# Kernel optimization log

Measured on AMD Instinct MI355X. Metric: run time of the kernel, lower is better.

The kernel has to match this reference:

```python
import jax, jax.numpy as jnp
import numpy as np

H = 2048      # hidden_size
NH = 32       # num attention heads
KVH = 8       # num kv heads
HD = 64       # head_dim
G = NH // KVH # kv groups (4)
EPS = 1e-6
THETA = 1000000.0


def _rms_norm(x, g):
    # normalize over last dim (head_dim)
    var = jnp.mean(jnp.square(x), axis=-1, keepdims=True)
    return x * jax.lax.rsqrt(var + EPS) * g


def _rope(seq_len, dtype):
    inv_freq = 1.0 / (THETA ** (jnp.arange(0, HD, 2, dtype=jnp.float32) / HD))
    pos = jnp.arange(seq_len, dtype=jnp.float32)
    freqs = pos[:, None] * inv_freq[None, :]          # [S, HD/2]
    emb = jnp.concatenate([freqs, freqs], axis=-1)    # [S, HD]
    return jnp.cos(emb).astype(dtype), jnp.sin(emb).astype(dtype)


def _rotate_half(x):
    x1, x2 = jnp.split(x, 2, axis=-1)
    return jnp.concatenate([-x2, x1], axis=-1)


def setup_inputs() -> dict:
    key = jax.random.key(0)
    ks = jax.random.split(key, 8)
    B, S = 1, 2048
    s = lambda fan_in: 1.0 / np.sqrt(fan_in)
    return {
        "hidden_states": jax.random.normal(ks[0], (B, S, H), jnp.float32),
        "Wq": jax.random.normal(ks[1], (H, NH * HD + NH), jnp.float32) * s(H),
        "Wk": jax.random.normal(ks[2], (H, KVH * HD), jnp.float32) * s(H),
        "Wv": jax.random.normal(ks[3], (H, KVH * HD), jnp.float32) * s(H),
        "Wo": jax.random.normal(ks[4], (NH * HD, H), jnp.float32) * s(NH * HD),
        "g_q": jnp.ones((HD,), jnp.float32),
        "g_k": jnp.ones((HD,), jnp.float32),
    }


def reference(hidden_states, Wq, Wk, Wv, Wo, g_q, g_k):
    B, S, _ = hidden_states.shape
    dtype = hidden_states.dtype

    qg = hidden_states @ Wq                              # [B,S,NH*HD+NH]
    k = hidden_states @ Wk                               # [B,S,KVH*HD]
    v = hidden_states @ Wv

    # headwise gate split, grouped per kv head (matches torch view/split)
    qg = qg.reshape(B, S, KVH, G * HD + G)
    q, gate = qg[..., : G * HD], qg[..., G * HD :]       # gate: [B,S,KVH,G]
    gate = gate.reshape(B, S, NH, 1)
    q = q.reshape(B, S, NH, HD).transpose(0, 2, 1, 3)    # [B,NH,S,HD]
    k = k.reshape(B, S, KVH, HD).transpose(0, 2, 1, 3)   # [B,KVH,S,HD]
    v = v.reshape(B, S, KVH, HD).transpose(0, 2, 1, 3)

    q = _rms_norm(q, g_q)
    k = _rms_norm(k, g_k)

    cos, sin = _rope(S, dtype)                           # [S,HD]
    cos, sin = cos[None, None], sin[None, None]
    q = q * cos + _rotate_half(q) * sin
    k = k * cos + _rotate_half(k) * sin

    # GQA: repeat kv heads
    k = jnp.repeat(k, G, axis=1)                         # [B,NH,S,HD]
    v = jnp.repeat(v, G, axis=1)

    # causal SDPA
    scale = 1.0 / np.sqrt(HD)
    scores = jnp.einsum("bhqd,bhkd->bhqk", q, k) * scale
    causal = jnp.tril(jnp.ones((S, S), bool))
    scores = jnp.where(causal[None, None], scores, jnp.finfo(dtype).min)
    probs = jax.nn.softmax(scores, axis=-1)
    attn = jnp.einsum("bhqk,bhkd->bhqd", probs, v)       # [B,NH,S,HD]

    attn = attn.transpose(0, 2, 1, 3)                    # [B,S,NH,HD]
    attn = attn * jax.nn.sigmoid(gate)
    attn = attn.reshape(B, S, NH * HD)
    return attn @ Wo
```

## Files before the change

kernel.cpp:

```cpp
#include <hip/hip_runtime.h>
#include <hip/hip_bf16.h>

#define SLEN 2048
#define HDIM 2048
#define NHEAD 32
#define KVHEAD 8
#define HEADD 64
#define NTOT 3104
#define NPAD 3200

typedef short bh8 __attribute__((ext_vector_type(8)));
typedef float f32x4 __attribute__((ext_vector_type(4)));

#define QSCALE 0.1803368801111204f

__device__ __forceinline__ unsigned short f2bf(float f) {
    union { float f; unsigned int u; } v; v.f = f;
    unsigned int u = v.u;
    return (unsigned short)((u + 0x7fffu + ((u >> 16) & 1u)) >> 16);
}

__device__ __forceinline__ unsigned int cvtpk_bf16(float lo, float hi) {
    unsigned int r;
    asm("v_cvt_pk_bf16_f32 %0, %1, %2" : "=v"(r) : "v"(lo), "v"(hi));
    return r;
}

__device__ __forceinline__ void gl_lds16(const unsigned short* g, unsigned short* l) {
    __builtin_amdgcn_global_load_lds(
        (const __attribute__((address_space(1))) unsigned int*)g,
        (__attribute__((address_space(3))) unsigned int*)l, 16, 0, 0);
}

__global__ void cast_x_k(const float* __restrict__ src, unsigned short* __restrict__ dst, int n) {
    int i = blockIdx.x * blockDim.x + threadIdx.x;
    int base = i * 4;
    if (base < n) {
        float4 f = *(const float4*)(src + base);
        ushort4 o;
        o.x = f2bf(f.x); o.y = f2bf(f.y); o.z = f2bf(f.z); o.w = f2bf(f.w);
        *(ushort4*)(dst + base) = o;
    }
}

__global__ void pack_wt_k(const float* __restrict__ Wq, const float* __restrict__ Wk,
                          const float* __restrict__ Wv, unsigned short* __restrict__ Wt) {
    __shared__ float tile[32][33];
    int n0 = blockIdx.x * 32, k0 = blockIdx.y * 32;
    int t = threadIdx.x;
    for (int i = 0; i < 4; i++) {
        int idx = i * 256 + t;
        int kr = idx >> 5, nc = idx & 31;
        int n = n0 + nc, k = k0 + kr;
        float val = 0.f;
        if (n < 2048)       { int h = n >> 6, d = n & 63; val = Wq[(size_t)k * 2080 + (h >> 2) * 260 + (h & 3) * 64 + d]; }
        else if (n < 2080)  { int h = n - 2048;           val = Wq[(size_t)k * 2080 + (h >> 2) * 260 + 256 + (h & 3)]; }
        else if (n < 2592)  { val = Wk[(size_t)k * 512 + (n - 2080)]; }
        else if (n < 3104)  { val = Wv[(size_t)k * 512 + (n - 2592)]; }
        tile[kr][nc] = val;
    }
    __syncthreads();
    for (int i = 0; i < 4; i++) {
        int idx = i * 256 + t;
        int nr = idx >> 5, kc = idx & 31;
        Wt[(size_t)(n0 + nr) * HDIM + (k0 + kc)] = f2bf(tile[kc][nr]);
    }
}

__global__ void pack_wot_k(const float* __restrict__ Wo, unsigned short* __restrict__ Wt) {
    __shared__ float tile[32][33];
    int n0 = blockIdx.x * 32, k0 = blockIdx.y * 32;
    int t = threadIdx.x;
    for (int i = 0; i < 4; i++) {
        int idx = i * 256 + t;
        int kr = idx >> 5, nc = idx & 31;
        tile[kr][nc] = Wo[(size_t)(k0 + kr) * 2048 + (n0 + nc)];
    }
    __syncthreads();
    for (int i = 0; i < 4; i++) {
        int idx = i * 256 + t;
        int nr = idx >> 5, kc = idx & 31;
        Wt[(size_t)(n0 + nr) * 2048 + (k0 + kc)] = f2bf(tile[kc][nr]);
    }
}

template<int NST>
__global__ __launch_bounds__(256) void gemm_nt64_k(const unsigned short* __restrict__ A,
                                                   const unsigned short* __restrict__ Bt,
                                                   float* __restrict__ C0,
                                                   float* __restrict__ C1,
                                                   int ldc, int mtiles, int ntiles) {
    const int K = 2048;
    __shared__ unsigned short As[3][64 * 32];
    __shared__ unsigned short Bs[3][128 * 32];
    int d = blockIdx.x;
    int nwg = gridDim.x;
    int cpx = nwg >> 3;
    int swz = (d & 7) * cpx + (d >> 3);
    int half = (swz >= ntiles) ? 1 : 0;
    int tile = swz - half * ntiles;
    int m0 = (tile % mtiles) * 64, n0 = (tile / mtiles) * 128;
    float* C = half ? C1 : C0;
    int koff = half * (NST * 32);
    int t = threadIdx.x;
    int w = t >> 6, l = t & 63;
    int wm = (w >> 1) * 32, wn = (w & 1) * 64;
    int lrow = l & 15, lc = l >> 4;
    int rsw = (lrow >> 1) & 3;
    int scol = ((l & 3) ^ ((l >> 3) & 3)) * 8;

    f32x4 acc[2][4];
    #pragma unroll
    for (int i = 0; i < 2; i++)
        #pragma unroll
        for (int j = 0; j < 4; j++)
            acc[i][j] = {0.f, 0.f, 0.f, 0.f};

    const unsigned short* ga = &A[(size_t)(m0 + w * 16 + (l >> 2)) * K + koff + scol];
    const unsigned short* gb = &Bt[(size_t)(n0 + w * 32 + (l >> 2)) * K + koff + scol];

#define STAGE_NT64(s, b) do { \
        gl_lds16(ga + (size_t)(s) * 32,                  &As[b][w * 512]); \
        gl_lds16(gb + (size_t)(s) * 32,                  &Bs[b][(w * 2 + 0) * 512]); \
        gl_lds16(gb + (size_t)(s) * 32 + 16 * (size_t)K, &Bs[b][(w * 2 + 1) * 512]); \
    } while (0)

#define GBODY(rb) do { \
        bh8 af[2], bb[4]; \
        _Pragma("unroll") \
        for (int i = 0; i < 2; i++) \
            af[i] = *(const bh8*)(&As[rb][(wm + i * 16 + lrow) * 32 + ((lc ^ rsw) * 8)]); \
        _Pragma("unroll") \
        for (int j = 0; j < 4; j++) \
            bb[j] = *(const bh8*)(&Bs[rb][(wn + j * 16 + lrow) * 32 + ((lc ^ rsw) * 8)]); \
        _Pragma("unroll") \
        for (int i = 0; i < 2; i++) \
            _Pragma("unroll") \
            for (int j = 0; j < 4; j++) \
                acc[i][j] = __builtin_amdgcn_mfma_f32_16x16x32_bf16(af[i], bb[j], acc[i][j], 0, 0, 0); \
    } while (0)

#define WB3 asm volatile("s_waitcnt vmcnt(3)\n\ts_barrier" ::: "memory")

    STAGE_NT64(0, 0);
    STAGE_NT64(1, 1);
    if constexpr (NST == 64) {
        for (int sb = 0; sb < 60; sb += 3) {
            WB3;
            STAGE_NT64(sb + 2, 2);
            GBODY(0);
            WB3;
            STAGE_NT64(sb + 3, 0);
            GBODY(1);
            WB3;
            STAGE_NT64(sb + 4, 1);
            GBODY(2);
        }
        WB3;
        STAGE_NT64(62, 2);
        GBODY(0);
        WB3;
        STAGE_NT64(63, 0);
        GBODY(1);
        WB3;
        GBODY(2);
        asm volatile("s_waitcnt vmcnt(0)\n\ts_barrier" ::: "memory");
        GBODY(0);
    } else {
        for (int sb = 0; sb < 30; sb += 3) {
            WB3;
            STAGE_NT64(sb + 2, 2);
            GBODY(0);
            WB3;
            STAGE_NT64(sb + 3, 0);
            GBODY(1);
            WB3;
            STAGE_NT64(sb + 4, 1);
            GBODY(2);
        }
        WB3;
        GBODY(0);
        asm volatile("s_waitcnt vmcnt(0)\n\ts_barrier" ::: "memory");
        GBODY(1);
    }
#undef WB3
#undef STAGE_NT64
#undef GBODY
    int col = l & 15, rbase = (l >> 4) * 4;
    for (int i = 0; i < 2; i++)
        for (int j = 0; j < 4; j++)
            #pragma unroll
            for (int r = 0; r < 4; r++)
                C[(size_t)(m0 + wm + i * 16 + rbase + r) * ldc + (n0 + wn + j * 16 + col)] = acc[i][j][r];
}

__global__ void addf4_k(const float* __restrict__ a, const float* __restrict__ b,
                        float* __restrict__ o) {
    int i = (blockIdx.x * 256 + threadIdx.x) * 4;
    float4 x = *(const float4*)(a + i);
    float4 y = *(const float4*)(b + i);
    float4 r; r.x = x.x + y.x; r.y = x.y + y.y; r.z = x.z + y.z; r.w = x.w + y.w;
    *(float4*)(o + i) = r;
}

__global__ void post_qkv_k(const float* __restrict__ QKVG,
                           unsigned short* __restrict__ Qr, unsigned short* __restrict__ Kr,
                           unsigned short* __restrict__ Vt, float* __restrict__ gate,
                           const float* __restrict__ g_q, const float* __restrict__ g_k) {
    __shared__ float tile[64][65];
    int b = blockIdx.x;
    if (b < 20480) {
        int wid = b * 4 + (threadIdx.x >> 6);
        int lane = threadIdx.x & 63;
        int type, s, hh;
        if (wid < SLEN * NHEAD) { type = 0; s = wid >> 5; hh = wid & 31; }
        else                    { int r = wid - SLEN * NHEAD; type = 1; s = r >> 3; hh = r & 7; }
        int col = (type == 0) ? hh * 64 + lane : 2080 + hh * 64 + lane;
        float x = QKVG[(size_t)s * NPAD + col];
        float sq = x * x;
        #pragma unroll
        for (int off = 32; off; off >>= 1) sq += __shfl_xor(sq, off);
        float inv = rsqrtf(sq * (1.f / 64.f) + 1e-6f);
        float g = (type == 0 ? g_q : g_k)[lane];
        float xn = x * inv * g;
        float xp = __shfl_xor(xn, 32);
        float xr = (lane < 32) ? -xp : xp;
        int i = lane & 31;
        float invf = __expf(-(float)i * (0.03125f * 13.815510557964274f));
        float ang = (float)s * invf;
        float c = cosf(ang), sn = sinf(ang);
        float r = xn * c + xr * sn;
        if (type == 0) Qr[((size_t)hh * SLEN + s) * 64 + lane] = f2bf(r * QSCALE);
        else           Kr[((size_t)hh * SLEN + s) * 64 + lane] = f2bf(r);
    } else if (b < 20736) {
        int b2 = b - 20480;
        int hh = b2 >> 5, s0 = (b2 & 31) * 64;
        int t = threadIdx.x;
        #pragma unroll
        for (int i = 0; i < 4; i++) {
            int idx = i * 256 + t;
            int sr = idx >> 4, c4 = (idx & 15) * 4;
            float4 f = *(const float4*)(&QKVG[(size_t)(s0 + sr) * NPAD + 2592 + hh * 64 + c4]);
            tile[sr][c4] = f.x; tile[sr][c4 + 1] = f.y; tile[sr][c4 + 2] = f.z; tile[sr][c4 + 3] = f.w;
        }
        __syncthreads();
        #pragma unroll
        for (int i = 0; i < 4; i++) {
            int idx = i * 256 + t;
            int dr = idx >> 4, c4 = (idx & 15) * 4;
            int hb = c4 >> 5, f = (c4 >> 4) & 1, g = (c4 >> 2) & 3;
            int p = (hb * 4 + g) * 8 + f * 4;
            ushort4 o;
            o.x = f2bf(tile[c4][dr]); o.y = f2bf(tile[c4 + 1][dr]);
            o.z = f2bf(tile[c4 + 2][dr]); o.w = f2bf(tile[c4 + 3][dr]);
            *(ushort4*)(&Vt[((size_t)hh * 64 + dr) * SLEN + s0 + p]) = o;
        }
    } else {
        int b2 = b - 20736;
        int i = b2 * 256 + threadIdx.x;
        int s = i >> 5, h = i & 31;
        float x = QKVG[(size_t)s * NPAD + 2048 + h];
        gate[i] = 1.f / (1.f + __expf(-x));
    }
}

__global__ __launch_bounds__(256) void attn_k(const unsigned short* __restrict__ Qr,
                                              const unsigned short* __restrict__ Kr,
                                              const unsigned short* __restrict__ Vt,
                                              const float* __restrict__ gate,
                                              unsigned short* __restrict__ attn) {
    __shared__ unsigned short Kls[3][64 * 64];
    __shared__ unsigned short Vls[3][64 * 64];
    int d = blockIdx.x;
    int kvh = d & 7;
    int h = kvh * 4 + ((d >> 3) & 3);
    int qt = 31 - (d >> 5);
    int t = threadIdx.x, w = t >> 6, l = t & 63;
    int ql = l & 15, g = l >> 4;
    const float NEGINF = -__builtin_inff();

    const unsigned short* Kh = Kr + (size_t)kvh * SLEN * 64;
    const unsigned short* Vh = Vt + (size_t)kvh * 64 * SLEN;
    const unsigned short* Qh = Qr + (size_t)h * SLEN * 64;
    int lk = g * 8;
    int r8 = l >> 3, c8 = l & 7;
    int cs = 8 * (c8 ^ r8);
    int R0 = w * 16, R1 = w * 16 + 8;
    int rdswz = (ql & 7) << 4;

    int q0 = qt * 64;
    int qrow = q0 + w * 16 + ql;

    bh8 qa0 = *(const bh8*)(Qh + (size_t)qrow * 64 + lk);
    bh8 qa1 = *(const bh8*)(Qh + (size_t)qrow * 64 + 32 + lk);

    f32x4 o[4];
    #pragma unroll
    for (int i = 0; i < 4; i++) o[i] = {0.f, 0.f, 0.f, 0.f};
    float m2 = NEGINF, lsum = 0.f;

    int ntiles = qt + 1;
    {
        gl_lds16(&Kh[(size_t)(0 + R0 + r8) * 64 + cs], &Kls[0][R0 * 64]);
        gl_lds16(&Kh[(size_t)(0 + R1 + r8) * 64 + cs], &Kls[0][R1 * 64]);
        gl_lds16(&Vh[(size_t)(R0 + r8) * SLEN + 0 + cs], &Vls[0][R0 * 64]);
        gl_lds16(&Vh[(size_t)(R1 + r8) * SLEN + 0 + cs], &Vls[0][R1 * 64]);
    }
    if (ntiles > 1) {
        gl_lds16(&Kh[(size_t)(64 + R0 + r8) * 64 + cs], &Kls[1][R0 * 64]);
        gl_lds16(&Kh[(size_t)(64 + R1 + r8) * 64 + cs], &Kls[1][R1 * 64]);
        gl_lds16(&Vh[(size_t)(R0 + r8) * SLEN + 64 + cs], &Vls[1][R0 * 64]);
        gl_lds16(&Vh[(size_t)(R1 + r8) * SLEN + 64 + cs], &Vls[1][R1 * 64]);
    }
    int rd = 0, wr = 2;

    for (int ti = 0; ti < ntiles; ti++) {
        if (ti + 1 < ntiles) asm volatile("s_waitcnt vmcnt(4)\n\ts_barrier" ::: "memory");
        else                 asm volatile("s_waitcnt vmcnt(0)\n\ts_barrier" ::: "memory");
        if (ti + 2 < ntiles) {
            int kv1 = (ti + 2) * 64;
            gl_lds16(&Kh[(size_t)(kv1 + R0 + r8) * 64 + cs], &Kls[wr][R0 * 64]);
            gl_lds16(&Kh[(size_t)(kv1 + R1 + r8) * 64 + cs], &Kls[wr][R1 * 64]);
            gl_lds16(&Vh[(size_t)(R0 + r8) * SLEN + kv1 + cs], &Vls[wr][R0 * 64]);
            gl_lds16(&Vh[(size_t)(R1 + r8) * SLEN + kv1 + cs], &Vls[wr][R1 * 64]);
        }
        const unsigned short* Kb = &Kls[rd][0];
        const unsigned short* Vb = &Vls[rd][0];
        int kv0 = ti * 64;
        f32x4 sct[4];
        __builtin_amdgcn_s_setprio(1);
        #pragma unroll
        for (int nt = 0; nt < 4; nt++) {
            int rb = (nt * 16 + ql) * 128;
            bh8 kb0 = *(const bh8*)(&Kb[(rb + ((g * 16) ^ rdswz)) >> 1]);
            bh8 kb1 = *(const bh8*)(&Kb[(rb + ((64 + g * 16) ^ rdswz)) >> 1]);
            f32x4 a = {0.f, 0.f, 0.f, 0.f};
            a = __builtin_amdgcn_mfma_f32_16x16x32_bf16(kb0, qa0, a, 0, 0, 0);
            a = __builtin_amdgcn_mfma_f32_16x16x32_bf16(kb1, qa1, a, 0, 0, 0);
            sct[nt] = a;
        }
        __builtin_amdgcn_s_setprio(0);
        if (ti == qt) {
            #pragma unroll
            for (int nt = 0; nt < 4; nt++)
                #pragma unroll
                for (int j = 0; j < 4; j++) {
                    int key = kv0 + nt * 16 + 4 * g + j;
                    if (key > qrow) sct[nt][j] = NEGINF;
                }
        }
        float mt0 = fmaxf(fmaxf(sct[0][0], sct[0][1]), fmaxf(sct[0][2], sct[0][3]));
        float mt1 = fmaxf(fmaxf(sct[1][0], sct[1][1]), fmaxf(sct[1][2], sct[1][3]));
        float mt2 = fmaxf(fmaxf(sct[2][0], sct[2][1]), fmaxf(sct[2][2], sct[2][3]));
        float mt3 = fmaxf(fmaxf(sct[3][0], sct[3][1]), fmaxf(sct[3][2], sct[3][3]));
        float mt = fmaxf(fmaxf(mt0, mt1), fmaxf(mt2, mt3));
        mt = fmaxf(mt, __shfl_xor(mt, 16));
        mt = fmaxf(mt, __shfl_xor(mt, 32));
        if (!__all(mt - m2 <= 8.f)) {
            float mnew = fmaxf(m2, mt);
            float resc = __builtin_amdgcn_exp2f(m2 - mnew);
            m2 = mnew;
            lsum *= resc;
            float rf[4];
            #pragma unroll
            for (int j = 0; j < 4; j++) rf[j] = __shfl(resc, 4 * g + j);
            #pragma unroll
            for (int nt = 0; nt < 4; nt++) {
                f32x4 oo = o[nt];
                #pragma unroll
                for (int j = 0; j < 4; j++) oo[j] *= rf[j];
                o[nt] = oo;
            }
        }
        float ps = 0.f;
        #pragma unroll
        for (int nt = 0; nt < 4; nt++)
            #pragma unroll
            for (int j = 0; j < 4; j++) {
                float p = __builtin_amdgcn_exp2f(sct[nt][j] - m2);
                sct[nt][j] = p;
                ps += p;
            }
        ps += __shfl_xor(ps, 16);
        ps += __shfl_xor(ps, 32);
        lsum += ps;
        union { unsigned int u[4]; bh8 v; } pa0, pa1;
        pa0.u[0] = cvtpk_bf16(sct[0][0], sct[0][1]);
        pa0.u[1] = cvtpk_bf16(sct[0][2], sct[0][3]);
        pa0.u[2] = cvtpk_bf16(sct[1][0], sct[1][1]);
        pa0.u[3] = cvtpk_bf16(sct[1][2], sct[1][3]);
        pa1.u[0] = cvtpk_bf16(sct[2][0], sct[2][1]);
        pa1.u[1] = cvtpk_bf16(sct[2][2], sct[2][3]);
        pa1.u[2] = cvtpk_bf16(sct[3][0], sct[3][1]);
        pa1.u[3] = cvtpk_bf16(sct[3][2], sct[3][3]);
        __builtin_amdgcn_s_setprio(1);
        #pragma unroll
        for (int nt = 0; nt < 4; nt++) {
            int rb = (nt * 16 + ql) * 128;
            bh8 vb0 = *(const bh8*)(&Vb[(rb + ((g * 16) ^ rdswz)) >> 1]);
            bh8 vb1 = *(const bh8*)(&Vb[(rb + ((64 + g * 16) ^ rdswz)) >> 1]);
            o[nt] = __builtin_amdgcn_mfma_f32_16x16x32_bf16(pa0.v, vb0, o[nt], 0, 0, 0);
            o[nt] = __builtin_amdgcn_mfma_f32_16x16x32_bf16(pa1.v, vb1, o[nt], 0, 0, 0);
        }
        __builtin_amdgcn_s_setprio(0);
        rd = (rd == 2) ? 0 : rd + 1;
        wr = (wr == 2) ? 0 : wr + 1;
    }

    float gf[4];
    #pragma unroll
    for (int j = 0; j < 4; j++) {
        float ls = __shfl(lsum, 4 * g + j);
        int row = q0 + w * 16 + 4 * g + j;
        gf[j] = gate[row * 32 + h] / ls;
    }
    #pragma unroll
    for (int j = 0; j < 4; j++) {
        int row = q0 + w * 16 + 4 * g + j;
        #pragma unroll
        for (int nt = 0; nt < 4; nt++)
            attn[(size_t)row * 2048 + h * 64 + nt * 16 + ql] = f2bf(o[nt][j] * gf[j]);
    }
}

extern "C" void kernel_launch(void* const* d_in, const int* in_sizes, int n_in,
                              void* d_out, int out_size, void* d_ws, size_t ws_size,
                              hipStream_t stream) {
    const float* hidden = (const float*)d_in[0];
    const float* Wq = (const float*)d_in[1];
    const float* Wk = (const float*)d_in[2];
    const float* Wv = (const float*)d_in[3];
    const float* Wo = (const float*)d_in[4];
    const float* gq = (const float*)d_in[5];
    const float* gk = (const float*)d_in[6];
    float* out = (float*)d_out;
    char* ws = (char*)d_ws;

    unsigned short* X     = (unsigned short*)(ws + 0);
    unsigned short* Wt    = (unsigned short*)(ws + 8388608);
    float*          QKVG  = (float*)(ws + 21495808);
    unsigned short* Qr    = (unsigned short*)(ws + 47710208);
    unsigned short* Kr    = (unsigned short*)(ws + 56098816);
    unsigned short* Vt    = (unsigned short*)(ws + 58195968);
    float*          gate  = (float*)(ws + 60293120);
    unsigned short* attnb = (unsigned short*)(ws + 60555264);
    unsigned short* Wot   = (unsigned short*)(ws + 68943872);
    float*          P1    = (float*)(ws + 77332480);
    float*          P0    = QKVG;

    cast_x_k<<<dim3(4096), dim3(256), 0, stream>>>(hidden, X, SLEN * HDIM);
    pack_wt_k<<<dim3(100, 64), dim3(256), 0, stream>>>(Wq, Wk, Wv, Wt);
    pack_wot_k<<<dim3(64, 64), dim3(256), 0, stream>>>(Wo, Wot);
    gemm_nt64_k<64><<<dim3(800), dim3(256), 0, stream>>>(X, Wt, QKVG, QKVG, NPAD, 32, 800);
    post_qkv_k<<<dim3(20992), dim3(256), 0, stream>>>(QKVG, Qr, Kr, Vt, gate, gq, gk);
    attn_k<<<dim3(1024), dim3(256), 0, stream>>>(Qr, Kr, Vt, gate, attnb);
    gemm_nt64_k<32><<<dim3(1024), dim3(256), 0, stream>>>(attnb, Wot, P0, P1, 2048, 32, 512);
    addf4_k<<<dim3(4096), dim3(256), 0, stream>>>(P0, P1, out);
}
```

Measured before the change: 169.9 us.

## Fuse QK RMSNorm, RoPE and gate sigmoid into QKV GEMM epilogue

Reorders the packed weight columns so Q, K, V and gate land on 128-wide tile boundaries. The QKV GEMM epilogue then applies RMSNorm, RoPE and scaling directly from accumulators and writes bf16 Q/K, and computes the gate sigmoid in place. Only V is still stored in fp32 and transposed by a smaller separate kernel. This removes the fp32 round trip of Q/K/gate through global memory and a large post-processing launch, at the cost of heavier epilogue work with scattered 2-byte stores and per-element sin/cos.

```diff
diff --git a/kernel.cpp b/kernel.cpp
--- a/kernel.cpp
+++ b/kernel.cpp
@@ -54,9 +54,9 @@
         int n = n0 + nc, k = k0 + kr;
         float val = 0.f;
         if (n < 2048)       { int h = n >> 6, d = n & 63; val = Wq[(size_t)k * 2080 + (h >> 2) * 260 + (h & 3) * 64 + d]; }
-        else if (n < 2080)  { int h = n - 2048;           val = Wq[(size_t)k * 2080 + (h >> 2) * 260 + 256 + (h & 3)]; }
-        else if (n < 2592)  { val = Wk[(size_t)k * 512 + (n - 2080)]; }
-        else if (n < 3104)  { val = Wv[(size_t)k * 512 + (n - 2592)]; }
+        else if (n < 2560)  { val = Wk[(size_t)k * 512 + (n - 2048)]; }
+        else if (n < 3072)  { val = Wv[(size_t)k * 512 + (n - 2560)]; }
+        else if (n < 3104)  { int h = n - 3072;           val = Wq[(size_t)k * 2080 + (h >> 2) * 260 + 256 + (h & 3)]; }
         tile[kr][nc] = val;
     }
     __syncthreads();
@@ -84,12 +84,17 @@
     }
 }
 
-template<int NST>
+template<int NST, bool FUSE>
 __global__ __launch_bounds__(256) void gemm_nt64_k(const unsigned short* __restrict__ A,
                                                    const unsigned short* __restrict__ Bt,
                                                    float* __restrict__ C0,
                                                    float* __restrict__ C1,
-                                                   int ldc, int mtiles, int ntiles) {
+                                                   int ldc, int mtiles, int ntiles,
+                                                   unsigned short* __restrict__ Qr,
+                                                   unsigned short* __restrict__ Kr,
+                                                   float* __restrict__ gate,
+                                                   const float* __restrict__ g_q,
+                                                   const float* __restrict__ g_k) {
     const int K = 2048;
     __shared__ unsigned short As[3][64 * 32];
     __shared__ unsigned short Bs[3][128 * 32];
@@ -187,11 +192,68 @@
 #undef STAGE_NT64
 #undef GBODY
     int col = l & 15, rbase = (l >> 4) * 4;
-    for (int i = 0; i < 2; i++)
-        for (int j = 0; j < 4; j++)
+    if constexpr (FUSE) {
+        int nt = n0 >> 7;
+        if (nt < 20) {
+            bool isQ = nt < 16;
+            int hd = ((n0 + wn) - (isQ ? 0 : 2048)) >> 6;
+            unsigned short* dst = (isQ ? Qr : Kr) + (size_t)hd * SLEN * 64;
+            const float* gv = isQ ? g_q : g_k;
+            float g0 = gv[col], g1 = gv[col + 16], g2 = gv[col + 32], g3 = gv[col + 48];
+            float invf0 = __expf(-(float)col * (0.03125f * 13.815510557964274f));
+            float invf1 = __expf(-(float)(col + 16) * (0.03125f * 13.815510557964274f));
+            float qs = isQ ? QSCALE : 1.0f;
             #pragma unroll
-            for (int r = 0; r < 4; r++)
-                C[(size_t)(m0 + wm + i * 16 + rbase + r) * ldc + (n0 + wn + j * 16 + col)] = acc[i][j][r];
+            for (int i = 0; i < 2; i++)
+                #pragma unroll
+                for (int r = 0; r < 4; r++) {
+                    int s = m0 + wm + i * 16 + rbase + r;
+                    float x0 = acc[i][0][r], x1 = acc[i][1][r];
+                    float x2 = acc[i][2][r], x3 = acc[i][3][r];
+                    float sq = x0 * x0 + x1 * x1 + x2 * x2 + x3 * x3;
+                    sq += __shfl_xor(sq, 1);
+                    sq += __shfl_xor(sq, 2);
+                    sq += __shfl_xor(sq, 4);
+                    sq += __shfl_xor(sq, 8);
+                    float inv = rsqrtf(sq * (1.f / 64.f) + 1e-6f);
+                    float xn0 = x0 * inv * g0, xn1 = x1 * inv * g1;
+                    float xn2 = x2 * inv * g2, xn3 = x3 * inv * g3;
+                    float a0 = (float)s * invf0, a1 = (float)s * invf1;
+                    float c0 = cosf(a0), sn0 = sinf(a0);
+                    float c1 = cosf(a1), sn1 = sinf(a1);
+                    unsigned short* dr = dst + (size_t)s * 64;
+                    dr[col]      = f2bf((xn0 * c0 - xn2 * sn0) * qs);
+                    dr[col + 16] = f2bf((xn1 * c1 - xn3 * sn1) * qs);
+                    dr[col + 32] = f2bf((xn2 * c0 + xn0 * sn0) * qs);
+                    dr[col + 48] = f2bf((xn3 * c1 + xn1 * sn1) * qs);
+                }
+        } else if (nt < 24) {
+            for (int i = 0; i < 2; i++)
+                for (int j = 0; j < 4; j++)
+                    #pragma unroll
+                    for (int r = 0; r < 4; r++)
+                        C[(size_t)(m0 + wm + i * 16 + rbase + r) * ldc + (n0 + wn + j * 16 + col)] = acc[i][j][r];
+        } else {
+            if (wn == 0) {
+                #pragma unroll
+                for (int i = 0; i < 2; i++)
+                    #pragma unroll
+                    for (int j = 0; j < 2; j++)
+                        #pragma unroll
+                        for (int r = 0; r < 4; r++) {
+                            int s = m0 + wm + i * 16 + rbase + r;
+                            int h = j * 16 + col;
+                            gate[s * 32 + h] = 1.f / (1.f + __expf(-acc[i][j][r]));
+                        }
+            }
+        }
+    } else {
+        for (int i = 0; i < 2; i++)
+            for (int j = 0; j < 4; j++)
+                #pragma unroll
+                for (int r = 0; r < 4; r++)
+                    C[(size_t)(m0 + wm + i * 16 + rbase + r) * ldc + (n0 + wn + j * 16 + col)] = acc[i][j][r];
+    }
 }
 
 __global__ void addf4_k(const float* __restrict__ a, const float* __restrict__ b,
@@ -203,64 +265,28 @@
     *(float4*)(o + i) = r;
 }
 
-__global__ void post_qkv_k(const float* __restrict__ QKVG,
-                           unsigned short* __restrict__ Qr, unsigned short* __restrict__ Kr,
-                           unsigned short* __restrict__ Vt, float* __restrict__ gate,
-                           const float* __restrict__ g_q, const float* __restrict__ g_k) {
+__global__ void vt_k(const float* __restrict__ QKVG, unsigned short* __restrict__ Vt) {
     __shared__ float tile[64][65];
-    int b = blockIdx.x;
-    if (b < 20480) {
-        int wid = b * 4 + (threadIdx.x >> 6);
-        int lane = threadIdx.x & 63;
-        int type, s, hh;
-        if (wid < SLEN * NHEAD) { type = 0; s = wid >> 5; hh = wid & 31; }
-        else                    { int r = wid - SLEN * NHEAD; type = 1; s = r >> 3; hh = r & 7; }
-        int col = (type == 0) ? hh * 64 + lane : 2080 + hh * 64 + lane;
-        float x = QKVG[(size_t)s * NPAD + col];
-        float sq = x * x;
-        #pragma unroll
-        for (int off = 32; off; off >>= 1) sq += __shfl_xor(sq, off);
-        float inv = rsqrtf(sq * (1.f / 64.f) + 1e-6f);
-        float g = (type == 0 ? g_q : g_k)[lane];
-        float xn = x * inv * g;
-        float xp = __shfl_xor(xn, 32);
-        float xr = (lane < 32) ? -xp : xp;
-        int i = lane & 31;
-        float invf = __expf(-(float)i * (0.03125f * 13.815510557964274f));
-        float ang = (float)s * invf;
-        float c = cosf(ang), sn = sinf(ang);
-        float r = xn * c + xr * sn;
-        if (type == 0) Qr[((size_t)hh * SLEN + s) * 64 + lane] = f2bf(r * QSCALE);
-        else           Kr[((size_t)hh * SLEN + s) * 64 + lane] = f2bf(r);
-    } else if (b < 20736) {
-        int b2 = b - 20480;
-        int hh = b2 >> 5, s0 = (b2 & 31) * 64;
-        int t = threadIdx.x;
-        #pragma unroll
-        for (int i = 0; i < 4; i++) {
-            int idx = i * 256 + t;
-            int sr = idx >> 4, c4 = (idx & 15) * 4;
-            float4 f = *(const float4*)(&QKVG[(size_t)(s0 + sr) * NPAD + 2592 + hh * 64 + c4]);
-            tile[sr][c4] = f.x; tile[sr][c4 + 1] = f.y; tile[sr][c4 + 2] = f.z; tile[sr][c4 + 3] = f.w;
-        }
-        __syncthreads();
-        #pragma unroll
-        for (int i = 0; i < 4; i++) {
-            int idx = i * 256 + t;
-            int dr = idx >> 4, c4 = (idx & 15) * 4;
-            int hb = c4 >> 5, f = (c4 >> 4) & 1, g = (c4 >> 2) & 3;
-            int p = (hb * 4 + g) * 8 + f * 4;
-            ushort4 o;
-            o.x = f2bf(tile[c4][dr]); o.y = f2bf(tile[c4 + 1][dr]);
-            o.z = f2bf(tile[c4 + 2][dr]); o.w = f2bf(tile[c4 + 3][dr]);
-            *(ushort4*)(&Vt[((size_t)hh * 64 + dr) * SLEN + s0 + p]) = o;
-        }
-    } else {
-        int b2 = b - 20736;
-        int i = b2 * 256 + threadIdx.x;
-        int s = i >> 5, h = i & 31;
-        float x = QKVG[(size_t)s * NPAD + 2048 + h];
-        gate[i] = 1.f / (1.f + __expf(-x));
+    int s0 = blockIdx.x * 64, hh = blockIdx.y;
+    int t = threadIdx.x;
+    #pragma unroll
+    for (int i = 0; i < 4; i++) {
+        int idx = i * 256 + t;
+        int sr = idx >> 4, c4 = (idx & 15) * 4;
+        float4 f = *(const float4*)(&QKVG[(size_t)(s0 + sr) * NPAD + 2560 + hh * 64 + c4]);
+        tile[sr][c4] = f.x; tile[sr][c4 + 1] = f.y; tile[sr][c4 + 2] = f.z; tile[sr][c4 + 3] = f.w;
+    }
+    __syncthreads();
+    #pragma unroll
+    for (int i = 0; i < 4; i++) {
+        int idx = i * 256 + t;
+        int dr = idx >> 4, c4 = (idx & 15) * 4;
+        int hb = c4 >> 5, f = (c4 >> 4) & 1, g = (c4 >> 2) & 3;
+        int p = (hb * 4 + g) * 8 + f * 4;
+        ushort4 o;
+        o.x = f2bf(tile[c4][dr]); o.y = f2bf(tile[c4 + 1][dr]);
+        o.z = f2bf(tile[c4 + 2][dr]); o.w = f2bf(tile[c4 + 3][dr]);
+        *(ushort4*)(&Vt[((size_t)hh * 64 + dr) * SLEN + s0 + p]) = o;
     }
 }
 
@@ -451,9 +477,11 @@
     cast_x_k<<<dim3(4096), dim3(256), 0, stream>>>(hidden, X, SLEN * HDIM);
     pack_wt_k<<<dim3(100, 64), dim3(256), 0, stream>>>(Wq, Wk, Wv, Wt);
     pack_wot_k<<<dim3(64, 64), dim3(256), 0, stream>>>(Wo, Wot);
-    gemm_nt64_k<64><<<dim3(800), dim3(256), 0, stream>>>(X, Wt, QKVG, QKVG, NPAD, 32, 800);
-    post_qkv_k<<<dim3(20992), dim3(256), 0, stream>>>(QKVG, Qr, Kr, Vt, gate, gq, gk);
+    gemm_nt64_k<64, true><<<dim3(800), dim3(256), 0, stream>>>(X, Wt, QKVG, QKVG, NPAD, 32, 800,
+                                                               Qr, Kr, gate, gq, gk);
+    vt_k<<<dim3(32, 8), dim3(256), 0, stream>>>(QKVG, Vt);
     attn_k<<<dim3(1024), dim3(256), 0, stream>>>(Qr, Kr, Vt, gate, attnb);
-    gemm_nt64_k<32><<<dim3(1024), dim3(256), 0, stream>>>(attnb, Wot, P0, P1, 2048, 32, 512);
+    gemm_nt64_k<32, false><<<dim3(1024), dim3(256), 0, stream>>>(attnb, Wot, P0, P1, 2048, 32, 512,
+                                                                 nullptr, nullptr, nullptr, nullptr, nullptr);
     addf4_k<<<dim3(4096), dim3(256), 0, stream>>>(P0, P1, out);
 }
```

Measured after the change: 160.1 us. 1.06x faster.
